# Kernel tuning notes

Hardware: AMD Instinct MI355X
Metric: run time of the kernel (lower is better)

Reference implementation:

```python
import jax, jax.numpy as jnp
import numpy as np

N_NODES = 10000
N_EDGES = 320000
MUL = 32            # multiplicity of each input/output irrep
RADIAL = 8          # edge scalar (radial basis) dim
HID = 64            # fc_neurons widths
NUM_NEIGHBORS = 32.0
MIX = np.pi / 8.0
INV_SQRT2 = 1.0 / np.sqrt(2.0)   # per-path alpha: 2 paths feed each mid irrep
INV_SQRT3 = 1.0 / np.sqrt(3.0)   # w3j(1,1,0) normalization


def setup_inputs() -> dict:
    key = jax.random.key(0)
    ks = jax.random.split(key, 16)
    inp = {
        "node_input": jax.random.normal(ks[0], (N_NODES, 4 * MUL), jnp.float32),  # 32x0e+32x1o flat
        "edge_attr": jax.random.normal(ks[1], (N_EDGES, 4), jnp.float32),          # 1x0e+1x1o (sh l=0,1)
        "edge_scalar_attr": jax.random.uniform(ks[2], (N_EDGES, RADIAL), jnp.float32),
        # first linear: 32x0e+32x1o -> (32x0e+32x1o) + (32x0e+32x1o); columns [:MUL]=conv path, [MUL:]=self path
        "W1_0e": jax.random.normal(ks[3], (MUL, 2 * MUL), jnp.float32),
        "W1_1o": jax.random.normal(ks[4], (MUL, 2 * MUL), jnp.float32),
        # radial MLP
        "W_mlp1": jax.random.normal(ks[5], (RADIAL, HID), jnp.float32),
        "W_mlp2": jax.random.normal(ks[6], (HID, HID), jnp.float32),
        # per-instruction 'uvu' path weights (mul_v = 1 squeezed): shape (HID, MUL)
        "Wp_00": jax.random.normal(ks[7], (HID, MUL), jnp.float32),  # 0e x 0e -> 0e
        "Wp_01": jax.random.normal(ks[8], (HID, MUL), jnp.float32),  # 0e x 1o -> 1o
        "Wp_10": jax.random.normal(ks[9], (HID, MUL), jnp.float32),  # 1o x 0e -> 1o
        "Wp_11": jax.random.normal(ks[10], (HID, MUL), jnp.float32), # 1o x 1o -> 0e
        # final linear: 64x0e+64x1o -> 32x0e+32x1o
        "W2_0e": jax.random.normal(ks[11], (2 * MUL, MUL), jnp.float32),
        "W2_1o": jax.random.normal(ks[12], (2 * MUL, MUL), jnp.float32),
        "edge_src": jax.random.randint(ks[13], (N_EDGES,), 0, N_NODES, jnp.int32),
        "edge_dst": jax.random.randint(ks[14], (N_EDGES,), 0, N_NODES, jnp.int32),
    }
    return inp


def _forward(node_input, edge_attr, edge_scalar_attr,
             W1_0e, W1_1o, W_mlp1, W_mlp2,
             Wp_00, Wp_01, Wp_10, Wp_11, W2_0e, W2_1o,
             edge_src, edge_dst):
    N = node_input.shape[0]
    # split flat node features into irrep blocks: 32x0e (N,32), 32x1o (N,32,3)
    x0 = node_input[:, :MUL]
    x1 = node_input[:, MUL:].reshape(N, MUL, 3)

    # ---- equivariant Linear: input -> input + output (fan-in normalized) ----
    f0 = (x0 @ W1_0e) / np.sqrt(MUL)                           # (N, 2*MUL)
    f1 = jnp.einsum('nui,uw->nwi', x1, W1_1o) / np.sqrt(MUL)   # (N, 2*MUL, 3)
    feat0, self0 = f0[:, :MUL], f0[:, MUL:]
    feat1, self1 = f1[:, :MUL], f1[:, MUL:]

    # ---- gather to edges ----
    e0 = feat0[edge_src]        # (E, MUL)
    e1 = feat1[edge_src]        # (E, MUL, 3)
    ea0 = edge_attr[:, :1]      # (E, 1) 0e
    ea1 = edge_attr[:, 1:4]     # (E, 3) 1o

    # ---- radial MLP -> per-edge per-path weights ----
    h = jax.nn.gelu((edge_scalar_attr @ W_mlp1) / np.sqrt(RADIAL))
    h = jax.nn.gelu((h @ W_mlp2) / np.sqrt(HID))               # (E, HID)
    w00 = h @ Wp_00   # (E, MUL)
    w01 = h @ Wp_01
    w10 = h @ Wp_10
    w11 = h @ Wp_11

    # ---- CG tensor product, 'uvu' mode (mul_v = 1) ----
    out0_a = w00 * e0 * ea0                                   # 0e x 0e -> 0e   (E, MUL)
    out0_b = w11 * jnp.sum(e1 * ea1[:, None, :], -1) * INV_SQRT3  # 1o.1o -> 0e
    out1_a = (w01 * e0)[:, :, None] * ea1[:, None, :]         # 0e x 1o -> 1o   (E, MUL, 3)
    out1_b = (w10[:, :, None] * e1) * ea0[:, :, None]         # 1o x 0e -> 1o
    mid0 = jnp.concatenate([out0_a, out0_b], axis=1) * INV_SQRT2  # (E, 2*MUL)   64x0e
    mid1 = jnp.concatenate([out1_a, out1_b], axis=1) * INV_SQRT2  # (E, 2*MUL, 3) 64x1o

    # ---- scatter-add to destination nodes ----
    n0 = jax.ops.segment_sum(mid0, edge_dst, num_segments=N) / np.sqrt(NUM_NEIGHBORS)
    n1 = jax.ops.segment_sum(mid1, edge_dst, num_segments=N) / np.sqrt(NUM_NEIGHBORS)

    # ---- final equivariant Linear: 64x0e+64x1o -> 32x0e+32x1o ----
    conv0 = (n0 @ W2_0e) / np.sqrt(2 * MUL)                    # (N, MUL)
    conv1 = jnp.einsum('nui,uw->nwi', n1, W2_1o) / np.sqrt(2 * MUL)  # (N, MUL, 3)

    c, s = np.cos(MIX), np.sin(MIX)
    y0 = c * self0 + s * conv0
    y1 = c * self1 + s * conv1
    return jnp.concatenate([y0, y1.reshape(N, MUL * 3)], axis=1)  # (N, 128)


def reference(node_input, edge_attr, edge_scalar_attr,
              W1_0e, W1_1o, W_mlp1, W_mlp2,
              Wp_00, Wp_01, Wp_10, Wp_11, W2_0e, W2_1o,
              edge_src, edge_dst):
    return _forward(node_input, edge_attr, edge_scalar_attr,
                    W1_0e, W1_1o, W_mlp1, W_mlp2,
                    Wp_00, Wp_01, Wp_10, Wp_11, W2_0e, W2_1o,
                    edge_src, edge_dst)
```

## Files before the change

kernel.cpp:

```cpp
#include <hip/hip_runtime.h>

typedef unsigned int uint32;
typedef unsigned short ushrt;
typedef __attribute__((ext_vector_type(4))) float f32x4;
typedef __attribute__((ext_vector_type(2))) float f32x2;
typedef __attribute__((ext_vector_type(8))) _Float16 halfx8;
typedef __attribute__((ext_vector_type(4))) uint32 uint32x4;

#define N_NODES 10000
#define N_EDGES 320000

#define SC_W1      0.17677669529663687f
#define SC_MLP1    0.35355339059327373f
#define SC_MLP2    0.125f
#define INV_SQRT3  0.5773502691896258f
#define COS_MIX    0.9238795325112867f
#define SIN_CONV   0.04783542904563623f

#define WS_FEATP 0
#define I_CNT    1280000
#define I_OFF    1290016
#define U_REC    1300032
#define U_WF     2580032
#define U_WBUF   2587200

__device__ __forceinline__ uint32 packh2(float a, float b) {
    _Float16 ha = (_Float16)a, hb = (_Float16)b;
    return (uint32)__builtin_bit_cast(unsigned short, ha) |
           ((uint32)__builtin_bit_cast(unsigned short, hb) << 16);
}
__device__ __forceinline__ unsigned short h16(float x) {
    _Float16 h = (_Float16)x;
    return __builtin_bit_cast(unsigned short, h);
}
__device__ __forceinline__ unsigned short pack_fp8_2(float a, float b) {
    return (unsigned short)(__builtin_amdgcn_cvt_pk_fp8_f32(a, b, 0, false) & 0xffff);
}
__device__ __forceinline__ float gelu_fast(float x) {
    float x2 = x * x;
    float z = x * __builtin_fmaf(0.03567740814f, x2, 0.7978845608f);
    float E = __builtin_amdgcn_exp2f(z * -2.885390082f);
    return x * __builtin_amdgcn_rcpf(1.0f + E);
}

#define K1_NODE_BLOCKS 2500
#define K1_CNT_BLOCKS  1250
#define K1_PREP_BLOCKS 7
__global__ __launch_bounds__(256) void k1_fused(
        const float* __restrict__ x,
        const float* __restrict__ W1_0e, const float* __restrict__ W1_1o,
        const int* __restrict__ edge_dst, int* __restrict__ cnt,
        const float* __restrict__ Wm1, const float* __restrict__ Wm2,
        const float* __restrict__ Wp00, const float* __restrict__ Wp01,
        const float* __restrict__ Wp10, const float* __restrict__ Wp11,
        uint32* __restrict__ wf,
        float* __restrict__ featp, float* __restrict__ out) {
    int b = blockIdx.x;
    if (b < K1_NODE_BLOCKS) {
        __shared__ float xrow[4][128];
        int wv = threadIdx.x >> 6, lane = threadIdx.x & 63;
        int node = b * 4 + wv;
        float2 v = *(const float2*)(x + (size_t)node * 128 + lane * 2);
        xrow[wv][lane * 2]     = v.x;
        xrow[wv][lane * 2 + 1] = v.y;
        __syncthreads();
        const float* sx = xrow[wv];
        int w = lane;
        float f0 = 0.f, f1x = 0.f, f1y = 0.f, f1z = 0.f;
#pragma unroll
        for (int u = 0; u < 32; ++u) {
            float w0 = W1_0e[u * 64 + w];
            float w1 = W1_1o[u * 64 + w];
            f0  += sx[u] * w0;
            f1x += sx[32 + u * 3 + 0] * w1;
            f1y += sx[32 + u * 3 + 1] * w1;
            f1z += sx[32 + u * 3 + 2] * w1;
        }
        f0 *= SC_W1; f1x *= SC_W1; f1y *= SC_W1; f1z *= SC_W1;
        if (w < 32) {
            featp[node * 128 + w]      = f0;
            featp[node * 128 + 32 + w] = f1x;
            featp[node * 128 + 64 + w] = f1y;
            featp[node * 128 + 96 + w] = f1z;
        } else {
            int ww = w - 32;
            out[node * 128 + ww] = COS_MIX * f0;
            out[node * 128 + 32 + ww * 3 + 0] = COS_MIX * f1x;
            out[node * 128 + 32 + ww * 3 + 1] = COS_MIX * f1y;
            out[node * 128 + 32 + ww * 3 + 2] = COS_MIX * f1z;
        }
    } else if (b < K1_NODE_BLOCKS + K1_CNT_BLOCKS) {
        int e = (b - K1_NODE_BLOCKS) * 256 + threadIdx.x;
        atomicAdd(&cnt[edge_dst[e]], 1);
    } else {
        int gid = (b - K1_NODE_BLOCKS - K1_CNT_BLOCKS) * 256 + threadIdx.x;
        int f = gid >> 6, lane = gid & 63;
        int kq = (lane >> 4) * 8;
        int c15 = lane & 15;
        float vals[8];
        if (f < 4) {
            int c = 16 * f + c15;
#pragma unroll
            for (int j = 0; j < 8; ++j) { int k = kq + j; vals[j] = (k < 8) ? Wm1[k * 64 + c] : 0.f; }
        } else if (f < 12) {
            int idx = f - 4, nt = idx >> 1, ks = idx & 1;
            int c = 16 * nt + c15;
#pragma unroll
            for (int j = 0; j < 8; ++j) { int k = 32 * ks + kq + j; vals[j] = Wm2[k * 64 + c]; }
        } else {
            int idx = f - 12, nt = idx >> 1, ks = idx & 1;
            int c = 16 * nt + c15;
            int u = c & 31, m = c >> 5;
            const float* W = (m == 0) ? Wp00 : (m == 1) ? Wp01 : (m == 2) ? Wp10 : Wp11;
            float sc = (m == 3) ? 0.125f * INV_SQRT3 : 0.125f;
#pragma unroll
            for (int j = 0; j < 8; ++j) { int k = 32 * ks + kq + j; vals[j] = W[k * 32 + u] * sc; }
        }
        uint32* o = wf + f * 256 + lane * 4;
#pragma unroll
        for (int w = 0; w < 4; ++w) o[w] = packh2(vals[2 * w], vals[2 * w + 1]);
    }
}

__global__ __launch_bounds__(1024) void csr_scan(const int* __restrict__ cnt,
                                                 int* __restrict__ off) {
    __shared__ int partial[1024];
    int t = threadIdx.x;
    const int CHUNK = 10;
    int base = t * CHUNK;
    int s = 0;
#pragma unroll
    for (int j = 0; j < CHUNK; ++j) {
        int idx = base + j;
        s += (idx < N_NODES) ? cnt[idx] : 0;
    }
    partial[t] = s;
    __syncthreads();
    for (int o = 1; o < 1024; o <<= 1) {
        int v = partial[t];
        int add = (t >= o) ? partial[t - o] : 0;
        __syncthreads();
        partial[t] = v + add;
        __syncthreads();
    }
    int run = (t > 0) ? partial[t - 1] : 0;
    for (int j = 0; j < CHUNK; ++j) {
        int idx = base + j;
        if (idx < N_NODES) {
            off[idx] = run;
            run += cnt[idx];
        }
    }
    if (t == 1023) off[N_NODES] = run;
}

#define MLP_BLOCKS 1250
__global__ __launch_bounds__(256) void mlp_scatter(
        const float* __restrict__ edge_scalar, const float* __restrict__ edge_attr,
        const int* __restrict__ src_in, const int* __restrict__ dst_in,
        int* __restrict__ off,
        const uint32* __restrict__ wf,
        uint32* __restrict__ wbuf, uint4* __restrict__ rec) {
    __shared__ unsigned short sh[4][1024];
    __shared__ uint32 ob[4][512];
    __shared__ float eaxs[4][16];
    __shared__ int   poss[4][16];
    int lane = threadIdx.x & 63;
    int wvq = threadIdx.x >> 6;
    int wave_id = blockIdx.x * 4 + wvq;
    int kq = (lane >> 4) * 8;
    int r15 = lane & 15;

    const uint32x4* wfp = (const uint32x4*)wf;
    halfx8 wb1[4], wb2[4][2], wbp[8][2];
#pragma unroll
    for (int nt = 0; nt < 4; ++nt)
        wb1[nt] = __builtin_bit_cast(halfx8, wfp[nt * 64 + lane]);
#pragma unroll
    for (int nt = 0; nt < 4; ++nt)
#pragma unroll
        for (int ks = 0; ks < 2; ++ks)
            wb2[nt][ks] = __builtin_bit_cast(halfx8, wfp[(4 + nt * 2 + ks) * 64 + lane]);
#pragma unroll
    for (int nt = 0; nt < 8; ++nt)
#pragma unroll
        for (int ks = 0; ks < 2; ++ks)
            wbp[nt][ks] = __builtin_bit_cast(halfx8, wfp[(12 + nt * 2 + ks) * 64 + lane]);

    const f32x4 z4 = {0.f, 0.f, 0.f, 0.f};
    unsigned short* shw = sh[wvq];
    uint32* obw = ob[wvq];
    unsigned short* obw16 = (unsigned short*)obw;

    for (int g = wave_id; g < N_EDGES / 16; g += MLP_BLOCKS * 4) {
        int e0 = g * 16;

        halfx8 a0 = (halfx8)0;
        if (lane < 16) {
            int e = e0 + lane;
            const float* esp = edge_scalar + (size_t)e * 8;
            float4 p = *(const float4*)esp;
            float4 q = *(const float4*)(esp + 4);
            float4 av = *(const float4*)(edge_attr + (size_t)e * 4);
            int dn = dst_in[e];
            int sn = src_in[e];
            int pos = atomicAdd(&off[dn], 1);
            poss[wvq][lane] = pos;
            eaxs[wvq][lane] = av.x;
            uint4 rv;
            rv.x = __float_as_uint(av.y);
            rv.y = __float_as_uint(av.z);
            rv.z = __float_as_uint(av.w);
            rv.w = (uint32)sn;
            rec[pos] = rv;
            a0[0] = (_Float16)p.x; a0[1] = (_Float16)p.y;
            a0[2] = (_Float16)p.z; a0[3] = (_Float16)p.w;
            a0[4] = (_Float16)q.x; a0[5] = (_Float16)q.y;
            a0[6] = (_Float16)q.z; a0[7] = (_Float16)q.w;
        }

        f32x4 acc1[4];
#pragma unroll
        for (int nt = 0; nt < 4; ++nt)
            acc1[nt] = __builtin_amdgcn_mfma_f32_16x16x32_f16(a0, wb1[nt], z4, 0, 0, 0);
#pragma unroll
        for (int nt = 0; nt < 4; ++nt)
#pragma unroll
            for (int i = 0; i < 4; ++i) {
                float gv = gelu_fast(acc1[nt][i] * SC_MLP1);
                int rr = (lane >> 4) * 4 + i;
                int ix = rr * 64 + 16 * nt + r15;
                shw[ix ^ ((rr & 7) << 3)] = h16(gv);
            }
        halfx8 a1[2];
#pragma unroll
        for (int ks = 0; ks < 2; ++ks) {
            int ix = r15 * 64 + 32 * ks + kq;
            a1[ks] = __builtin_bit_cast(halfx8,
                       *(const uint32x4*)&shw[ix ^ ((r15 & 7) << 3)]);
        }

        f32x4 acc2[4];
#pragma unroll
        for (int nt = 0; nt < 4; ++nt) {
            acc2[nt] = __builtin_amdgcn_mfma_f32_16x16x32_f16(a1[0], wb2[nt][0], z4, 0, 0, 0);
            acc2[nt] = __builtin_amdgcn_mfma_f32_16x16x32_f16(a1[1], wb2[nt][1], acc2[nt], 0, 0, 0);
        }
#pragma unroll
        for (int nt = 0; nt < 4; ++nt)
#pragma unroll
            for (int i = 0; i < 4; ++i) {
                float gv = gelu_fast(acc2[nt][i] * SC_MLP2);
                int rr = (lane >> 4) * 4 + i;
                int ix = rr * 64 + 16 * nt + r15;
                shw[ix ^ ((rr & 7) << 3)] = h16(gv);
            }
        halfx8 a2[2];
#pragma unroll
        for (int ks = 0; ks < 2; ++ks) {
            int ix = r15 * 64 + 32 * ks + kq;
            a2[ks] = __builtin_bit_cast(halfx8,
                       *(const uint32x4*)&shw[ix ^ ((r15 & 7) << 3)]);
        }

        f32x4 accp[8];
#pragma unroll
        for (int nt = 0; nt < 8; ++nt) {
            accp[nt] = __builtin_amdgcn_mfma_f32_16x16x32_f16(a2[0], wbp[nt][0], z4, 0, 0, 0);
            accp[nt] = __builtin_amdgcn_mfma_f32_16x16x32_f16(a2[1], wbp[nt][1], accp[nt], 0, 0, 0);
        }

#pragma unroll
        for (int i = 0; i < 4; ++i) {
            int rr = (lane >> 4) * 4 + i;
            float eax = eaxs[wvq][rr];
            unsigned short* orow = obw16 + rr * 64;
            orow[r15]      = pack_fp8_2(accp[0][i] * eax, accp[2][i]);
            orow[16 + r15] = pack_fp8_2(accp[1][i] * eax, accp[3][i]);
            orow[32 + r15] = pack_fp8_2(accp[4][i] * eax, accp[6][i]);
            orow[48 + r15] = pack_fp8_2(accp[5][i] * eax, accp[7][i]);
        }
#pragma unroll
        for (int pass = 0; pass < 2; ++pass) {
            int r = pass * 8 + (lane >> 3);
            int pos = poss[wvq][r];
            int c4 = (lane & 7) * 4;
            uint32x4 v = *(const uint32x4*)&obw[r * 32 + c4];
            *(uint32x4*)(wbuf + (size_t)pos * 32 + c4) = v;
        }
    }
}

__global__ __launch_bounds__(256) void gather(const int* __restrict__ off,
                                              const int* __restrict__ cnt,
                                              const uint4* __restrict__ rec,
                                              const uint32* __restrict__ wbuf,
                                              const float* __restrict__ featp,
                                              const float* __restrict__ W2_0e,
                                              const float* __restrict__ W2_1o,
                                              float* __restrict__ out) {
    int wv = threadIdx.x >> 6;
    int lane = threadIdx.x & 63;
    int node = blockIdx.x * 4 + wv;
    int u = lane & 31;
    int half = lane >> 5;

    int end = __builtin_amdgcn_readfirstlane(off[node]);
    int beg = end - __builtin_amdgcn_readfirstlane(cnt[node]);

    float a0acc = 0.f, a1x = 0.f, a1y = 0.f, a1z = 0.f;
    int offA = u + half * 32, offB = 64 + u, offC = 96 + u;
    const ushrt* wbuf16 = (const ushrt*)wbuf;
    int uslot = (half << 5) + u;

    for (int i0 = beg; i0 < end; i0 += 64) {
        int nn = end - i0;
        if (nn > 64) nn = 64;
        int idx = i0 + ((lane < nn) ? lane : 0);
        uint4 rv = rec[idx];
        int eyv = (int)rv.x, ezv = (int)rv.y, ewv = (int)rv.z, svv = (int)rv.w;
        for (int j0 = 0; j0 < nn; j0 += 4) {
            uint32 wl_[4];
            float fa_[4], fb_[4], fc_[4], ey_[4], ez_[4], ew_[4];
#pragma unroll
            for (int t = 0; t < 4; ++t) {
                int j = j0 + t;
                int jc = (j < nn) ? j : nn - 1;
                ey_[t] = __uint_as_float((uint32)__builtin_amdgcn_readlane(eyv, jc));
                ez_[t] = __uint_as_float((uint32)__builtin_amdgcn_readlane(ezv, jc));
                ew_[t] = __uint_as_float((uint32)__builtin_amdgcn_readlane(ewv, jc));
                int s  = __builtin_amdgcn_readlane(svv, jc);
                uint32 wl = (uint32)wbuf16[(size_t)(i0 + jc) * 64 + uslot];
                wl_[t] = (j < nn) ? wl : 0u;
                const float* fp = featp + (size_t)s * 128;
                fa_[t] = fp[offA];
                fb_[t] = fp[offB];
                fc_[t] = fp[offC];
            }
#pragma unroll
            for (int t = 0; t < 4; ++t) {
                f32x2 wab = __builtin_amdgcn_cvt_pk_f32_fp8((int)wl_[t], false);
                float wa = wab.x;
                float wb = wab.y;
                float va = half ? ey_[t] : 1.0f;
                float vb = half ? ez_[t] : 0.0f;
                float vc = half ? ew_[t] : 0.0f;
                float dot = fa_[t] * va + fb_[t] * vb + fc_[t] * vc;
                float w0s = half ? wb : wa;
                a0acc += w0s * dot;
                float m  = half ? wa : wb * fa_[t];
                float vx = half ? fa_[t] : ey_[t];
                float vy = half ? fb_[t] : ez_[t];
                float vz = half ? fc_[t] : ew_[t];
                a1x += m * vx; a1y += m * vy; a1z += m * vz;
            }
        }
    }

    __shared__ float red[4][256];
    float* r = red[wv];
    int c = (half << 5) + u;
    r[c] = a0acc;
    int b = 64 + c * 3;
    r[b] = a1x; r[b + 1] = a1y; r[b + 2] = a1z;
    __syncthreads();

    if (half == 0) {
        float acc = 0.f;
#pragma unroll 8
        for (int w = 0; w < 64; ++w) acc += r[w] * W2_0e[w * 32 + u];
        int o = node * 128 + u;
        out[o] = out[o] + SIN_CONV * acc;
    } else {
        float c0 = 0.f, c1 = 0.f, c2 = 0.f;
#pragma unroll 8
        for (int w = 0; w < 64; ++w) {
            float bw = W2_1o[w * 32 + u];
            c0 += r[64 + w * 3 + 0] * bw;
            c1 += r[64 + w * 3 + 1] * bw;
            c2 += r[64 + w * 3 + 2] * bw;
        }
        int o = node * 128 + 32 + u * 3;
        out[o + 0] = out[o + 0] + SIN_CONV * c0;
        out[o + 1] = out[o + 1] + SIN_CONV * c1;
        out[o + 2] = out[o + 2] + SIN_CONV * c2;
    }
}

extern "C" void kernel_launch(void* const* d_in, const int* in_sizes, int n_in,
                              void* d_out, int out_size, void* d_ws, size_t ws_size,
                              hipStream_t stream) {
    const float* node_input  = (const float*)d_in[0];
    const float* edge_attr   = (const float*)d_in[1];
    const float* edge_scalar = (const float*)d_in[2];
    const float* W1_0e       = (const float*)d_in[3];
    const float* W1_1o       = (const float*)d_in[4];
    const float* W_mlp1      = (const float*)d_in[5];
    const float* W_mlp2      = (const float*)d_in[6];
    const float* Wp00        = (const float*)d_in[7];
    const float* Wp01        = (const float*)d_in[8];
    const float* Wp10        = (const float*)d_in[9];
    const float* Wp11        = (const float*)d_in[10];
    const float* W2_0e       = (const float*)d_in[11];
    const float* W2_1o       = (const float*)d_in[12];
    const int*   edge_src    = (const int*)d_in[13];
    const int*   edge_dst    = (const int*)d_in[14];
    float* ws   = (float*)d_ws;
    int*   wsI  = (int*)d_ws;
    uint32* wsU = (uint32*)d_ws;
    uint4* recp = (uint4*)(wsU + U_REC);
    float* outp = (float*)d_out;

    hipMemsetAsync(wsI + I_CNT, 0, (N_NODES + 1) * sizeof(int), stream);

    k1_fused<<<K1_NODE_BLOCKS + K1_CNT_BLOCKS + K1_PREP_BLOCKS, 256, 0, stream>>>(
        node_input, W1_0e, W1_1o, edge_dst, wsI + I_CNT,
        W_mlp1, W_mlp2, Wp00, Wp01, Wp10, Wp11, wsU + U_WF, ws + WS_FEATP, outp);
    csr_scan<<<1, 1024, 0, stream>>>(wsI + I_CNT, wsI + I_OFF);
    mlp_scatter<<<MLP_BLOCKS, 256, 0, stream>>>(edge_scalar, edge_attr,
                                                edge_src, edge_dst, wsI + I_OFF,
                                                wsU + U_WF, wsU + U_WBUF, recp);
    gather<<<N_NODES / 4, 256, 0, stream>>>(wsI + I_OFF, wsI + I_CNT, recp,
                                            wsU + U_WBUF, ws + WS_FEATP,
                                            W2_0e, W2_1o, outp);
}
```

Baseline: 121.5 us.

## Move node linear from count kernel into edge MLP/scatter kernel

Moves the per-node first equivariant linear (featp and self-path output) out of the first fused kernel, which also counts edges and prepares weights, and into the edge MLP/scatter kernel as extra trailing blocks. The first kernel now only counts edges and packs weights, so the serial chain memset→count→scan reaches the scan sooner. The node work then overlaps with the MLP edge work. The cost is that the merged kernel carries the extra xrow shared memory and branch in every block, which may lower occupancy for the MLP blocks.

```diff
diff --git a/kernel.cpp b/kernel.cpp
--- a/kernel.cpp
+++ b/kernel.cpp
@@ -43,28 +43,107 @@
     return x * __builtin_amdgcn_rcpf(1.0f + E);
 }
 
-#define K1_NODE_BLOCKS 2500
 #define K1_CNT_BLOCKS  1250
 #define K1_PREP_BLOCKS 7
 __global__ __launch_bounds__(256) void k1_fused(
-        const float* __restrict__ x,
-        const float* __restrict__ W1_0e, const float* __restrict__ W1_1o,
         const int* __restrict__ edge_dst, int* __restrict__ cnt,
         const float* __restrict__ Wm1, const float* __restrict__ Wm2,
         const float* __restrict__ Wp00, const float* __restrict__ Wp01,
         const float* __restrict__ Wp10, const float* __restrict__ Wp11,
-        uint32* __restrict__ wf,
+        uint32* __restrict__ wf) {
+    int b = blockIdx.x;
+    if (b < K1_CNT_BLOCKS) {
+        int e = b * 256 + threadIdx.x;
+        atomicAdd(&cnt[edge_dst[e]], 1);
+    } else {
+        int gid = (b - K1_CNT_BLOCKS) * 256 + threadIdx.x;
+        int f = gid >> 6, lane = gid & 63;
+        int kq = (lane >> 4) * 8;
+        int c15 = lane & 15;
+        float vals[8];
+        if (f < 4) {
+            int c = 16 * f + c15;
+#pragma unroll
+            for (int j = 0; j < 8; ++j) { int k = kq + j; vals[j] = (k < 8) ? Wm1[k * 64 + c] : 0.f; }
+        } else if (f < 12) {
+            int idx = f - 4, nt = idx >> 1, ks = idx & 1;
+            int c = 16 * nt + c15;
+#pragma unroll
+            for (int j = 0; j < 8; ++j) { int k = 32 * ks + kq + j; vals[j] = Wm2[k * 64 + c]; }
+        } else {
+            int idx = f - 12, nt = idx >> 1, ks = idx & 1;
+            int c = 16 * nt + c15;
+            int u = c & 31, m = c >> 5;
+            const float* W = (m == 0) ? Wp00 : (m == 1) ? Wp01 : (m == 2) ? Wp10 : Wp11;
+            float sc = (m == 3) ? 0.125f * INV_SQRT3 : 0.125f;
+#pragma unroll
+            for (int j = 0; j < 8; ++j) { int k = 32 * ks + kq + j; vals[j] = W[k * 32 + u] * sc; }
+        }
+        uint32* o = wf + f * 256 + lane * 4;
+#pragma unroll
+        for (int w = 0; w < 4; ++w) o[w] = packh2(vals[2 * w], vals[2 * w + 1]);
+    }
+}
+
+__global__ __launch_bounds__(1024) void csr_scan(const int* __restrict__ cnt,
+                                                 int* __restrict__ off) {
+    __shared__ int partial[1024];
+    int t = threadIdx.x;
+    const int CHUNK = 10;
+    int base = t * CHUNK;
+    int s = 0;
+#pragma unroll
+    for (int j = 0; j < CHUNK; ++j) {
+        int idx = base + j;
+        s += (idx < N_NODES) ? cnt[idx] : 0;
+    }
+    partial[t] = s;
+    __syncthreads();
+    for (int o = 1; o < 1024; o <<= 1) {
+        int v = partial[t];
+        int add = (t >= o) ? partial[t - o] : 0;
+        __syncthreads();
+        partial[t] = v + add;
+        __syncthreads();
+    }
+    int run = (t > 0) ? partial[t - 1] : 0;
+    for (int j = 0; j < CHUNK; ++j) {
+        int idx = base + j;
+        if (idx < N_NODES) {
+            off[idx] = run;
+            run += cnt[idx];
+        }
+    }
+    if (t == 1023) off[N_NODES] = run;
+}
+
+#define MLP_BLOCKS 1250
+#define K3_NODE_BLOCKS 2500
+__global__ __launch_bounds__(256) void k3_fused(
+        const float* __restrict__ edge_scalar, const float* __restrict__ edge_attr,
+        const int* __restrict__ src_in, const int* __restrict__ dst_in,
+        int* __restrict__ off,
+        const uint32* __restrict__ wf,
+        uint32* __restrict__ wbuf, uint4* __restrict__ rec,
+        const float* __restrict__ x,
+        const float* __restrict__ W1_0e, const float* __restrict__ W1_1o,
         float* __restrict__ featp, float* __restrict__ out) {
-    int b = blockIdx.x;
-    if (b < K1_NODE_BLOCKS) {
-        __shared__ float xrow[4][128];
-        int wv = threadIdx.x >> 6, lane = threadIdx.x & 63;
-        int node = b * 4 + wv;
+    __shared__ unsigned short sh[4][1024];
+    __shared__ uint32 ob[4][512];
+    __shared__ float eaxs[4][16];
+    __shared__ int   poss[4][16];
+    __shared__ float xrow[4][128];
+
+    int lane = threadIdx.x & 63;
+    int wvq = threadIdx.x >> 6;
+
+    if (blockIdx.x >= MLP_BLOCKS) {
+        int node = (blockIdx.x - MLP_BLOCKS) * 4 + wvq;
         float2 v = *(const float2*)(x + (size_t)node * 128 + lane * 2);
-        xrow[wv][lane * 2]     = v.x;
-        xrow[wv][lane * 2 + 1] = v.y;
+        xrow[wvq][lane * 2]     = v.x;
+        xrow[wvq][lane * 2 + 1] = v.y;
         __syncthreads();
-        const float* sx = xrow[wv];
+        const float* sx = xrow[wvq];
         int w = lane;
         float f0 = 0.f, f1x = 0.f, f1y = 0.f, f1z = 0.f;
 #pragma unroll
@@ -89,84 +168,9 @@
             out[node * 128 + 32 + ww * 3 + 1] = COS_MIX * f1y;
             out[node * 128 + 32 + ww * 3 + 2] = COS_MIX * f1z;
         }
-    } else if (b < K1_NODE_BLOCKS + K1_CNT_BLOCKS) {
-        int e = (b - K1_NODE_BLOCKS) * 256 + threadIdx.x;
-        atomicAdd(&cnt[edge_dst[e]], 1);
-    } else {
-        int gid = (b - K1_NODE_BLOCKS - K1_CNT_BLOCKS) * 256 + threadIdx.x;
-        int f = gid >> 6, lane = gid & 63;
-        int kq = (lane >> 4) * 8;
-        int c15 = lane & 15;
-        float vals[8];
-        if (f < 4) {
-            int c = 16 * f + c15;
-#pragma unroll
-            for (int j = 0; j < 8; ++j) { int k = kq + j; vals[j] = (k < 8) ? Wm1[k * 64 + c] : 0.f; }
-        } else if (f < 12) {
-            int idx = f - 4, nt = idx >> 1, ks = idx & 1;
-            int c = 16 * nt + c15;
-#pragma unroll
-            for (int j = 0; j < 8; ++j) { int k = 32 * ks + kq + j; vals[j] = Wm2[k * 64 + c]; }
-        } else {
-            int idx = f - 12, nt = idx >> 1, ks = idx & 1;
-            int c = 16 * nt + c15;
-            int u = c & 31, m = c >> 5;
-            const float* W = (m == 0) ? Wp00 : (m == 1) ? Wp01 : (m == 2) ? Wp10 : Wp11;
-            float sc = (m == 3) ? 0.125f * INV_SQRT3 : 0.125f;
-#pragma unroll
-            for (int j = 0; j < 8; ++j) { int k = 32 * ks + kq + j; vals[j] = W[k * 32 + u] * sc; }
-        }
-        uint32* o = wf + f * 256 + lane * 4;
-#pragma unroll
-        for (int w = 0; w < 4; ++w) o[w] = packh2(vals[2 * w], vals[2 * w + 1]);
-    }
-}
-
-__global__ __launch_bounds__(1024) void csr_scan(const int* __restrict__ cnt,
-                                                 int* __restrict__ off) {
-    __shared__ int partial[1024];
-    int t = threadIdx.x;
-    const int CHUNK = 10;
-    int base = t * CHUNK;
-    int s = 0;
-#pragma unroll
-    for (int j = 0; j < CHUNK; ++j) {
-        int idx = base + j;
-        s += (idx < N_NODES) ? cnt[idx] : 0;
-    }
-    partial[t] = s;
-    __syncthreads();
-    for (int o = 1; o < 1024; o <<= 1) {
-        int v = partial[t];
-        int add = (t >= o) ? partial[t - o] : 0;
-        __syncthreads();
-        partial[t] = v + add;
-        __syncthreads();
-    }
-    int run = (t > 0) ? partial[t - 1] : 0;
-    for (int j = 0; j < CHUNK; ++j) {
-        int idx = base + j;
-        if (idx < N_NODES) {
-            off[idx] = run;
-            run += cnt[idx];
-        }
-    }
-    if (t == 1023) off[N_NODES] = run;
-}
-
-#define MLP_BLOCKS 1250
-__global__ __launch_bounds__(256) void mlp_scatter(
-        const float* __restrict__ edge_scalar, const float* __restrict__ edge_attr,
-        const int* __restrict__ src_in, const int* __restrict__ dst_in,
-        int* __restrict__ off,
-        const uint32* __restrict__ wf,
-        uint32* __restrict__ wbuf, uint4* __restrict__ rec) {
-    __shared__ unsigned short sh[4][1024];
-    __shared__ uint32 ob[4][512];
-    __shared__ float eaxs[4][16];
-    __shared__ int   poss[4][16];
-    int lane = threadIdx.x & 63;
-    int wvq = threadIdx.x >> 6;
+        return;
+    }
+
     int wave_id = blockIdx.x * 4 + wvq;
     int kq = (lane >> 4) * 8;
     int r15 = lane & 15;
@@ -413,13 +417,14 @@
 
     hipMemsetAsync(wsI + I_CNT, 0, (N_NODES + 1) * sizeof(int), stream);
 
-    k1_fused<<<K1_NODE_BLOCKS + K1_CNT_BLOCKS + K1_PREP_BLOCKS, 256, 0, stream>>>(
-        node_input, W1_0e, W1_1o, edge_dst, wsI + I_CNT,
-        W_mlp1, W_mlp2, Wp00, Wp01, Wp10, Wp11, wsU + U_WF, ws + WS_FEATP, outp);
+    k1_fused<<<K1_CNT_BLOCKS + K1_PREP_BLOCKS, 256, 0, stream>>>(
+        edge_dst, wsI + I_CNT,
+        W_mlp1, W_mlp2, Wp00, Wp01, Wp10, Wp11, wsU + U_WF);
     csr_scan<<<1, 1024, 0, stream>>>(wsI + I_CNT, wsI + I_OFF);
-    mlp_scatter<<<MLP_BLOCKS, 256, 0, stream>>>(edge_scalar, edge_attr,
-                                                edge_src, edge_dst, wsI + I_OFF,
-                                                wsU + U_WF, wsU + U_WBUF, recp);
+    k3_fused<<<MLP_BLOCKS + K3_NODE_BLOCKS, 256, 0, stream>>>(
+        edge_scalar, edge_attr, edge_src, edge_dst, wsI + I_OFF,
+        wsU + U_WF, wsU + U_WBUF, recp,
+        node_input, W1_0e, W1_1o, ws + WS_FEATP, outp);
     gather<<<N_NODES / 4, 256, 0, stream>>>(wsI + I_OFF, wsI + I_CNT, recp,
                                             wsU + U_WBUF, ws + WS_FEATP,
                                             W2_0e, W2_1o, outp);
```

Measured after the change: 120.0 us. No clear change (-1.3%).
